# Kernel tuning notes

Hardware: AMD Instinct MI355X
Metric: run time of the kernel (lower is better)

## Reference

```python
import jax, jax.numpy as jnp
import numpy as np

D_MODEL = 1024
N_HEADS = 16
HEAD_DIM = D_MODEL // N_HEADS


def setup_inputs() -> dict:
    key = jax.random.key(0)
    k1, k2, k3 = jax.random.split(key, 3)
    x = jax.random.normal(k1, (4, 2048, D_MODEL), dtype=jnp.float32)
    # per-head qkv Linear (bias=False): torch weight [3*head_dim, d_model];
    # store transposed and stacked over heads: [H, d_model, 3*head_dim]
    w_qkv = jax.random.normal(k2, (N_HEADS, D_MODEL, 3 * HEAD_DIM), dtype=jnp.float32) * (1.0 / np.sqrt(D_MODEL))
    # output Linear (bias=False), stored transposed: [d_model, d_model]
    w_out = jax.random.normal(k3, (D_MODEL, D_MODEL), dtype=jnp.float32) * (1.0 / np.sqrt(D_MODEL))
    return {"x": x, "w_qkv": w_qkv, "w_out": w_out}


def reference(x, w_qkv, w_out):
    hd = HEAD_DIM
    # all heads' qkv in one contraction: [B, H, S, 3*hd]
    qkv = jnp.einsum("bsd,hde->bhse", x, w_qkv)
    q, k, v = qkv[..., :hd], qkv[..., hd:2 * hd], qkv[..., 2 * hd:]
    scale = 1.0 / hd  # NOTE: original scales by 1/dk, not 1/sqrt(dk)
    scores = jnp.einsum("bhqe,bhke->bhqk", q, k) * scale
    attn = jax.nn.softmax(scores, axis=-1)
    z = jnp.einsum("bhqk,bhke->bhqe", attn, v)  # [B, H, S, hd]
    # concat heads along feature dim (head order = list order)
    b, h, s, _ = z.shape
    z = jnp.transpose(z, (0, 2, 1, 3)).reshape(b, s, h * hd)
    return z @ w_out
```

## Files before the change

kernel.cpp:

```cpp
#include <hip/hip_runtime.h>
#include <hip/hip_bf16.h>

typedef unsigned short u16;
typedef __attribute__((ext_vector_type(4))) float f32x4;
typedef __attribute__((ext_vector_type(16))) float f32x16;
typedef __attribute__((ext_vector_type(8))) short s16x8;
typedef __attribute__((ext_vector_type(4))) unsigned short u16x4;

static __device__ __forceinline__ u16 f32_to_bf16(float f) {
    union { float f; unsigned u; } v; v.f = f;
    unsigned r = v.u + 0x7FFF + ((v.u >> 16) & 1);
    return (u16)(r >> 16);
}

static __device__ __forceinline__ unsigned cvt_pk_bf16(float lo, float hi) {
    unsigned r;
    asm("v_cvt_pk_bf16_f32 %0, %1, %2" : "=v"(r) : "v"(lo), "v"(hi));
    return r;
}

static __device__ __forceinline__ void pswap2(unsigned &a, unsigned &b) {
#if defined(__has_builtin) && __has_builtin(__builtin_amdgcn_permlane32_swap)
    auto r = __builtin_amdgcn_permlane32_swap(a, b, false, false);
    a = r[0]; b = r[1];
#else
    asm volatile("v_permlane32_swap_b32 %0, %1" : "+v"(a), "+v"(b));
#endif
}

static __device__ __forceinline__ float xhalf_sum(float x) {
    unsigned a = __float_as_uint(x), b = a;
    pswap2(a, b);
    return __uint_as_float(a) + __uint_as_float(b);
}

static __device__ __forceinline__ float fexp2(float x) {
#if defined(__has_builtin) && __has_builtin(__builtin_amdgcn_exp2f)
    return __builtin_amdgcn_exp2f(x);
#else
    return exp2f(x);
#endif
}

#define GLOAD_LDS16(gptr, lptr) \
    __builtin_amdgcn_global_load_lds((const __attribute__((address_space(1))) void*)(gptr), \
                                     (__attribute__((address_space(3))) void*)(lptr), 16, 0, 0)


__global__ void cvt_f32_bf16(const float* __restrict__ in, u16* __restrict__ out, int n) {
    int i = (blockIdx.x * 256 + threadIdx.x) * 4;
    if (i + 3 < n) {
        f32x4 v = *(const f32x4*)(in + i);
        u16x4 o;
        o.x = f32_to_bf16(v.x); o.y = f32_to_bf16(v.y);
        o.z = f32_to_bf16(v.z); o.w = f32_to_bf16(v.w);
        *(u16x4*)(out + i) = o;
    }
}

__global__ void cvt_wqkvT(const float* __restrict__ w, u16* __restrict__ wt) {
    int tid = blockIdx.x * 256 + threadIdx.x;
    int k = tid & 1023, n = tid >> 10;
    int h = n / 192, e = n - h * 192;
    wt[tid] = f32_to_bf16(w[(h * 1024 + k) * 192 + e]);
}

__global__ void cvt_woutT(const float* __restrict__ w, u16* __restrict__ wt) {
    int tid = blockIdx.x * 256 + threadIdx.x;
    int k = tid & 1023, n = tid >> 10;
    wt[tid] = f32_to_bf16(w[k * 1024 + n]);
}


template <int EPI>
__global__ __launch_bounds__(256, 4)
void gemm_bt(const u16* __restrict__ A, const u16* __restrict__ B,
             float* __restrict__ Cf, u16* __restrict__ Qb, u16* __restrict__ Kb,
             u16* __restrict__ Vt, int M, int N, int K) {
    __shared__ __align__(16) u16 lA[2][128 * 32];
    __shared__ __align__(16) u16 lB[2][128 * 32];

    const int t = threadIdx.x;
    const int lane = t & 63;
    const int wave = t >> 6;
    const int wr = wave >> 1, wc = wave & 1;
    const int l15 = lane & 15, g = lane >> 4;

    const int nwg = gridDim.x;
    const int cpx = nwg >> 3;
    const int orig = blockIdx.x;
    const int logical = (orig & 7) * cpx + (orig >> 3);

    const int nbx = N >> 7;
    const int bx = logical % nbx, by = logical / nbx;
    const int bm = by << 7, bn = bx << 7;

    f32x4 acc[4][4] = {};

    const int sr0 = t >> 2;
    const int ss  = t & 3;

    const u16* Abase = A + (size_t)bm * K;
    const u16* Bbase = B + (size_t)bn * K;

#define GSTAGE(buf, kt) do { \
    _Pragma("unroll") \
    for (int c = 0; c < 2; ++c) { \
        int r = sr0 + 64 * c; \
        int cl = ss ^ (r & 3); \
        GLOAD_LDS16(Abase + (size_t)r * K + (kt) + cl * 8, &lA[buf][(r * 4 + ss) * 8]); \
        GLOAD_LDS16(Bbase + (size_t)r * K + (kt) + cl * 8, &lB[buf][(r * 4 + ss) * 8]); \
    } } while (0)

    GSTAGE(0, 0);

    const int NT = K >> 5;
    for (int ti = 0; ti < NT; ++ti) {
        __syncthreads();
        if (ti + 1 < NT) GSTAGE((ti + 1) & 1, (ti + 1) << 5);

        const u16* Ac = lA[ti & 1];
        const u16* Bc = lB[ti & 1];
        s16x8 a[4], b[4];
#pragma unroll
        for (int i = 0; i < 4; ++i) {
            int r = wr * 64 + i * 16 + l15;
            int sl = g ^ (r & 3);
            a[i] = *(const s16x8*)&Ac[(r * 4 + sl) * 8];
        }
#pragma unroll
        for (int j = 0; j < 4; ++j) {
            int r = wc * 64 + j * 16 + l15;
            int sl = g ^ (r & 3);
            b[j] = *(const s16x8*)&Bc[(r * 4 + sl) * 8];
        }
#pragma unroll
        for (int i = 0; i < 4; ++i)
#pragma unroll
            for (int j = 0; j < 4; ++j)
                acc[i][j] = __builtin_amdgcn_mfma_f32_16x16x32_bf16(b[j], a[i], acc[i][j], 0, 0, 0);
    }
#undef GSTAGE

    if constexpr (EPI == 0) {
#pragma unroll
        for (int i = 0; i < 4; ++i) {
            int m = bm + wr * 64 + i * 16 + l15;
#pragma unroll
            for (int j = 0; j < 4; ++j) {
                int n0 = bn + wc * 64 + j * 16 + g * 4;
                *(f32x4*)&Cf[(size_t)m * N + n0] = acc[i][j];
            }
        }
    } else {
        const float qscale = 0.022542110013890054f;
#pragma unroll
        for (int j = 0; j < 4; ++j) {
            int n0 = bn + wc * 64 + j * 16 + g * 4;
            int h = n0 / 192;
            int e0 = n0 - h * 192;
#pragma unroll
            for (int i = 0; i < 4; ++i) {
                int m = bm + wr * 64 + i * 16 + l15;
                int bb = m >> 11, s = m & 2047;
                int bh = bb * 16 + h;
                if (e0 < 64) {
                    u16x4 q;
#pragma unroll
                    for (int r = 0; r < 4; ++r) q[r] = f32_to_bf16(acc[i][j][r] * qscale);
                    *(u16x4*)&Qb[((size_t)bh * 2048 + s) * 64 + e0] = q;
                } else if (e0 < 128) {
                    u16x4 kk;
#pragma unroll
                    for (int r = 0; r < 4; ++r) kk[r] = f32_to_bf16(acc[i][j][r]);
                    *(u16x4*)&Kb[((size_t)bh * 2048 + s) * 64 + (e0 - 64)] = kk;
                } else {
#pragma unroll
                    for (int r = 0; r < 4; ++r)
                        Vt[((size_t)bh * 64 + (e0 - 128 + r)) * 2048 + s] = f32_to_bf16(acc[i][j][r]);
                }
            }
        }
    }
}

__global__ __launch_bounds__(512, 4)
void attn32(const u16* __restrict__ Qb, const u16* __restrict__ Kb,
            const u16* __restrict__ Vt, u16* __restrict__ Zb) {
    __shared__ __align__(16) u16 lK[2][64 * 64];
    __shared__ __align__(16) u16 lV[2][64 * 64];
    __shared__ float lds_l[8][32];

    const int t = threadIdx.x;
    const int lane = t & 63;
    const int w = t >> 6;
    const int l31 = lane & 31, hi = lane >> 5;
    const int r7 = l31 & 7;

    const int orig = blockIdx.x;
    const int logical = (orig & 7) * 64 + (orig >> 3);
    const int bh = logical >> 3;
    const int qt = logical & 7;
    const int q0 = qt * 256 + w * 32;

    const u16* Kbh = Kb + (size_t)bh * 2048 * 64;
    const u16* Vbh = Vt + (size_t)bh * 64 * 2048;

    const int lr = lane >> 3;
    const int lc = (lane & 7) ^ lr;

    const u16* Qp = Qb + ((size_t)bh * 2048 + q0 + l31) * 64 + hi * 8;
    s16x8 qf[4];
#pragma unroll
    for (int kd = 0; kd < 4; ++kd) qf[kd] = *(const s16x8*)(Qp + kd * 16);

    f32x16 o0 = {}, o1 = {};
    float l = 0.f;

#define STAGE(buf, kvn) do { \
    int gr = w * 8 + lr; \
    GLOAD_LDS16(Kbh + (size_t)((kvn) + gr) * 64 + lc * 8, \
                &lK[buf][w * 512 + lane * 8]); \
    GLOAD_LDS16(Vbh + (size_t)gr * 2048 + (kvn) + lc * 8, \
                &lV[buf][w * 512 + lane * 8]); \
    } while (0)

    STAGE(0, 0);
    __syncthreads();

#pragma unroll 2
    for (int ti = 0; ti < 32; ++ti) {
        const int cur = ti & 1;
        const int kvn = ((ti + 1) & 31) * 64;

        STAGE(cur ^ 1, kvn);

        const u16* Kc = &lK[cur][0];
        f32x16 p0 = {}, p1 = {};
        __builtin_amdgcn_s_setprio(1);
#pragma unroll
        for (int kd = 0; kd < 4; ++kd) {
            int cs = ((hi + 2 * kd) ^ r7) * 8;
            s16x8 kf0 = *(const s16x8*)&Kc[l31 * 64 + cs];
            p0 = __builtin_amdgcn_mfma_f32_32x32x16_bf16(kf0, qf[kd], p0, 0, 0, 0);
            s16x8 kf1 = *(const s16x8*)&Kc[(l31 + 32) * 64 + cs];
            p1 = __builtin_amdgcn_mfma_f32_32x32x16_bf16(kf1, qf[kd], p1, 0, 0, 0);
        }
        __builtin_amdgcn_s_setprio(0);

        float rs0 = 0.f, rs1 = 0.f, rs2 = 0.f, rs3 = 0.f;
#pragma unroll
        for (int r = 0; r < 16; r += 4) {
            p0[r]     = fexp2(p0[r]);     rs0 += p0[r];
            p0[r + 1] = fexp2(p0[r + 1]); rs1 += p0[r + 1];
            p0[r + 2] = fexp2(p0[r + 2]); rs2 += p0[r + 2];
            p0[r + 3] = fexp2(p0[r + 3]); rs3 += p0[r + 3];
            p1[r]     = fexp2(p1[r]);     rs0 += p1[r];
            p1[r + 1] = fexp2(p1[r + 1]); rs1 += p1[r + 1];
            p1[r + 2] = fexp2(p1[r + 2]); rs2 += p1[r + 2];
            p1[r + 3] = fexp2(p1[r + 3]); rs3 += p1[r + 3];
        }
        l += xhalf_sum((rs0 + rs1) + (rs2 + rs3));

        union { unsigned u[8]; s16x8 v[2]; } pa0, pa1;
        {
            unsigned c0 = cvt_pk_bf16(p0[0],  p0[1]);
            unsigned c1 = cvt_pk_bf16(p0[2],  p0[3]);
            unsigned c2 = cvt_pk_bf16(p0[4],  p0[5]);
            unsigned c3 = cvt_pk_bf16(p0[6],  p0[7]);
            unsigned c4 = cvt_pk_bf16(p0[8],  p0[9]);
            unsigned c5 = cvt_pk_bf16(p0[10], p0[11]);
            unsigned c6 = cvt_pk_bf16(p0[12], p0[13]);
            unsigned c7 = cvt_pk_bf16(p0[14], p0[15]);
            pswap2(c0, c2); pswap2(c1, c3);
            pswap2(c4, c6); pswap2(c5, c7);
            pa0.u[0] = c0; pa0.u[1] = c1; pa0.u[2] = c2; pa0.u[3] = c3;
            pa0.u[4] = c4; pa0.u[5] = c5; pa0.u[6] = c6; pa0.u[7] = c7;
        }
        {
            unsigned c0 = cvt_pk_bf16(p1[0],  p1[1]);
            unsigned c1 = cvt_pk_bf16(p1[2],  p1[3]);
            unsigned c2 = cvt_pk_bf16(p1[4],  p1[5]);
            unsigned c3 = cvt_pk_bf16(p1[6],  p1[7]);
            unsigned c4 = cvt_pk_bf16(p1[8],  p1[9]);
            unsigned c5 = cvt_pk_bf16(p1[10], p1[11]);
            unsigned c6 = cvt_pk_bf16(p1[12], p1[13]);
            unsigned c7 = cvt_pk_bf16(p1[14], p1[15]);
            pswap2(c0, c2); pswap2(c1, c3);
            pswap2(c4, c6); pswap2(c5, c7);
            pa1.u[0] = c0; pa1.u[1] = c1; pa1.u[2] = c2; pa1.u[3] = c3;
            pa1.u[4] = c4; pa1.u[5] = c5; pa1.u[6] = c6; pa1.u[7] = c7;
        }

        const u16* Vc = &lV[cur][0];
        __builtin_amdgcn_s_setprio(1);
#pragma unroll
        for (int ks = 0; ks < 4; ++ks) {
            s16x8 pav = (ks < 2) ? pa0.v[ks & 1] : pa1.v[ks & 1];
            int cs = ((hi + 2 * ks) ^ r7) * 8;
            s16x8 vf0 = *(const s16x8*)&Vc[l31 * 64 + cs];
            o0 = __builtin_amdgcn_mfma_f32_32x32x16_bf16(pav, vf0, o0, 0, 0, 0);
            s16x8 vf1 = *(const s16x8*)&Vc[(l31 + 32) * 64 + cs];
            o1 = __builtin_amdgcn_mfma_f32_32x32x16_bf16(pav, vf1, o1, 0, 0, 0);
        }
        __builtin_amdgcn_s_setprio(0);

        __syncthreads();
    }
#undef STAGE

    if (lane < 32) lds_l[w][l31] = l;
    __syncthreads();

    const int b = bh >> 4, h = bh & 15;
#pragma unroll
    for (int r = 0; r < 16; ++r) {
        int qrow = (r & 3) + 8 * (r >> 2) + 4 * hi;
        float inv = 1.0f / lds_l[w][qrow];
        size_t rowbase = ((size_t)(b * 2048 + q0 + qrow)) * 1024 + h * 64 + l31;
        Zb[rowbase]      = f32_to_bf16(o0[r] * inv);
        Zb[rowbase + 32] = f32_to_bf16(o1[r] * inv);
    }
}


extern "C" void kernel_launch(void* const* d_in, const int* in_sizes, int n_in,
                              void* d_out, int out_size, void* d_ws, size_t ws_size,
                              hipStream_t stream) {
    const float* x     = (const float*)d_in[0];
    const float* w_qkv = (const float*)d_in[1];
    const float* w_out = (const float*)d_in[2];
    float* out = (float*)d_out;

    char* ws = (char*)d_ws;
    u16* xb  = (u16*)ws; ws += (size_t)8192 * 1024 * 2;
    u16* wqT = (u16*)ws; ws += (size_t)3072 * 1024 * 2;
    u16* woT = (u16*)ws; ws += (size_t)1024 * 1024 * 2;
    u16* Qb  = (u16*)ws; ws += (size_t)64 * 2048 * 64 * 2;
    u16* Kb  = (u16*)ws; ws += (size_t)64 * 2048 * 64 * 2;
    u16* Vt  = (u16*)ws; ws += (size_t)64 * 2048 * 64 * 2;
    u16* Zb  = (u16*)ws; ws += (size_t)8192 * 1024 * 2;

    cvt_f32_bf16<<<dim3(8192), dim3(256), 0, stream>>>(x, xb, 8192 * 1024);
    cvt_wqkvT<<<dim3(12288), dim3(256), 0, stream>>>(w_qkv, wqT);
    cvt_woutT<<<dim3(4096), dim3(256), 0, stream>>>(w_out, woT);

    gemm_bt<1><<<dim3(64 * 24), dim3(256), 0, stream>>>(xb, wqT, nullptr, Qb, Kb, Vt,
                                                        8192, 3072, 1024);
    attn32<<<dim3(512), dim3(512), 0, stream>>>(Qb, Kb, Vt, Zb);
    gemm_bt<0><<<dim3(64 * 8), dim3(256), 0, stream>>>(Zb, woT, out, nullptr, nullptr, nullptr,
                                                       8192, 1024, 1024);
}
```

Before: 210.6 us.

## Use 128-wide KV tiles and compute softmax row sums via ones-matrix MFMA

```diff
diff --git a/kernel.cpp b/kernel.cpp
--- a/kernel.cpp
+++ b/kernel.cpp
@@ -26,12 +26,6 @@
 #else
     asm volatile("v_permlane32_swap_b32 %0, %1" : "+v"(a), "+v"(b));
 #endif
-}
-
-static __device__ __forceinline__ float xhalf_sum(float x) {
-    unsigned a = __float_as_uint(x), b = a;
-    pswap2(a, b);
-    return __uint_as_float(a) + __uint_as_float(b);
 }
 
 static __device__ __forceinline__ float fexp2(float x) {
@@ -187,9 +181,8 @@
 __global__ __launch_bounds__(512, 4)
 void attn32(const u16* __restrict__ Qb, const u16* __restrict__ Kb,
             const u16* __restrict__ Vt, u16* __restrict__ Zb) {
-    __shared__ __align__(16) u16 lK[2][64 * 64];
-    __shared__ __align__(16) u16 lV[2][64 * 64];
-    __shared__ float lds_l[8][32];
+    __shared__ __align__(16) u16 lK[2][128 * 64];
+    __shared__ __align__(16) u16 lV[2][64 * 128];
 
     const int t = threadIdx.x;
     const int lane = t & 63;
@@ -206,118 +199,125 @@
     const u16* Kbh = Kb + (size_t)bh * 2048 * 64;
     const u16* Vbh = Vt + (size_t)bh * 64 * 2048;
 
-    const int lr = lane >> 3;
-    const int lc = (lane & 7) ^ lr;
-
     const u16* Qp = Qb + ((size_t)bh * 2048 + q0 + l31) * 64 + hi * 8;
     s16x8 qf[4];
 #pragma unroll
     for (int kd = 0; kd < 4; ++kd) qf[kd] = *(const s16x8*)(Qp + kd * 16);
 
-    f32x16 o0 = {}, o1 = {};
-    float l = 0.f;
+    s16x8 ones;
+#pragma unroll
+    for (int i = 0; i < 8; ++i) ones[i] = (short)0x3F80;
+
+    f32x16 o0 = {}, o1 = {}, ol = {};
 
 #define STAGE(buf, kvn) do { \
-    int gr = w * 8 + lr; \
-    GLOAD_LDS16(Kbh + (size_t)((kvn) + gr) * 64 + lc * 8, \
-                &lK[buf][w * 512 + lane * 8]); \
-    GLOAD_LDS16(Vbh + (size_t)gr * 2048 + (kvn) + lc * 8, \
-                &lV[buf][w * 512 + lane * 8]); \
-    } while (0)
+    _Pragma("unroll") \
+    for (int j = 0; j < 2; ++j) { \
+        int kr = w * 16 + j * 8 + (lane >> 3); \
+        GLOAD_LDS16(Kbh + (size_t)((kvn) + kr) * 64 + ((lane & 7) ^ (lane >> 3)) * 8, \
+                    &lK[buf][w * 1024 + j * 512 + lane * 8]); \
+        int vr = w * 8 + j * 4 + (lane >> 4); \
+        int vcl = (lane & 15) ^ (j * 4 + (lane >> 4)); \
+        GLOAD_LDS16(Vbh + (size_t)vr * 2048 + (kvn) + vcl * 8, \
+                    &lV[buf][w * 1024 + j * 512 + lane * 8]); \
+    } } while (0)
 
     STAGE(0, 0);
     __syncthreads();
 
 #pragma unroll 2
-    for (int ti = 0; ti < 32; ++ti) {
+    for (int ti = 0; ti < 16; ++ti) {
         const int cur = ti & 1;
-        const int kvn = ((ti + 1) & 31) * 64;
+        const int kvn = ((ti + 1) & 15) * 128;
 
         STAGE(cur ^ 1, kvn);
 
         const u16* Kc = &lK[cur][0];
-        f32x16 p0 = {}, p1 = {};
-        __builtin_amdgcn_s_setprio(1);
-#pragma unroll
-        for (int kd = 0; kd < 4; ++kd) {
-            int cs = ((hi + 2 * kd) ^ r7) * 8;
-            s16x8 kf0 = *(const s16x8*)&Kc[l31 * 64 + cs];
-            p0 = __builtin_amdgcn_mfma_f32_32x32x16_bf16(kf0, qf[kd], p0, 0, 0, 0);
-            s16x8 kf1 = *(const s16x8*)&Kc[(l31 + 32) * 64 + cs];
-            p1 = __builtin_amdgcn_mfma_f32_32x32x16_bf16(kf1, qf[kd], p1, 0, 0, 0);
-        }
-        __builtin_amdgcn_s_setprio(0);
-
-        float rs0 = 0.f, rs1 = 0.f, rs2 = 0.f, rs3 = 0.f;
-#pragma unroll
-        for (int r = 0; r < 16; r += 4) {
-            p0[r]     = fexp2(p0[r]);     rs0 += p0[r];
-            p0[r + 1] = fexp2(p0[r + 1]); rs1 += p0[r + 1];
-            p0[r + 2] = fexp2(p0[r + 2]); rs2 += p0[r + 2];
-            p0[r + 3] = fexp2(p0[r + 3]); rs3 += p0[r + 3];
-            p1[r]     = fexp2(p1[r]);     rs0 += p1[r];
-            p1[r + 1] = fexp2(p1[r + 1]); rs1 += p1[r + 1];
-            p1[r + 2] = fexp2(p1[r + 2]); rs2 += p1[r + 2];
-            p1[r + 3] = fexp2(p1[r + 3]); rs3 += p1[r + 3];
-        }
-        l += xhalf_sum((rs0 + rs1) + (rs2 + rs3));
-
-        union { unsigned u[8]; s16x8 v[2]; } pa0, pa1;
-        {
-            unsigned c0 = cvt_pk_bf16(p0[0],  p0[1]);
-            unsigned c1 = cvt_pk_bf16(p0[2],  p0[3]);
-            unsigned c2 = cvt_pk_bf16(p0[4],  p0[5]);
-            unsigned c3 = cvt_pk_bf16(p0[6],  p0[7]);
-            unsigned c4 = cvt_pk_bf16(p0[8],  p0[9]);
-            unsigned c5 = cvt_pk_bf16(p0[10], p0[11]);
-            unsigned c6 = cvt_pk_bf16(p0[12], p0[13]);
-            unsigned c7 = cvt_pk_bf16(p0[14], p0[15]);
-            pswap2(c0, c2); pswap2(c1, c3);
-            pswap2(c4, c6); pswap2(c5, c7);
-            pa0.u[0] = c0; pa0.u[1] = c1; pa0.u[2] = c2; pa0.u[3] = c3;
-            pa0.u[4] = c4; pa0.u[5] = c5; pa0.u[6] = c6; pa0.u[7] = c7;
-        }
-        {
-            unsigned c0 = cvt_pk_bf16(p1[0],  p1[1]);
-            unsigned c1 = cvt_pk_bf16(p1[2],  p1[3]);
-            unsigned c2 = cvt_pk_bf16(p1[4],  p1[5]);
-            unsigned c3 = cvt_pk_bf16(p1[6],  p1[7]);
-            unsigned c4 = cvt_pk_bf16(p1[8],  p1[9]);
-            unsigned c5 = cvt_pk_bf16(p1[10], p1[11]);
-            unsigned c6 = cvt_pk_bf16(p1[12], p1[13]);
-            unsigned c7 = cvt_pk_bf16(p1[14], p1[15]);
-            pswap2(c0, c2); pswap2(c1, c3);
-            pswap2(c4, c6); pswap2(c5, c7);
-            pa1.u[0] = c0; pa1.u[1] = c1; pa1.u[2] = c2; pa1.u[3] = c3;
-            pa1.u[4] = c4; pa1.u[5] = c5; pa1.u[6] = c6; pa1.u[7] = c7;
-        }
-
         const u16* Vc = &lV[cur][0];
-        __builtin_amdgcn_s_setprio(1);
-#pragma unroll
-        for (int ks = 0; ks < 4; ++ks) {
-            s16x8 pav = (ks < 2) ? pa0.v[ks & 1] : pa1.v[ks & 1];
-            int cs = ((hi + 2 * ks) ^ r7) * 8;
-            s16x8 vf0 = *(const s16x8*)&Vc[l31 * 64 + cs];
-            o0 = __builtin_amdgcn_mfma_f32_32x32x16_bf16(pav, vf0, o0, 0, 0, 0);
-            s16x8 vf1 = *(const s16x8*)&Vc[(l31 + 32) * 64 + cs];
-            o1 = __builtin_amdgcn_mfma_f32_32x32x16_bf16(pav, vf1, o1, 0, 0, 0);
-        }
-        __builtin_amdgcn_s_setprio(0);
+
+#pragma unroll
+        for (int hs = 0; hs < 2; ++hs) {
+            f32x16 p0 = {}, p1 = {};
+            __builtin_amdgcn_s_setprio(1);
+#pragma unroll
+            for (int kd = 0; kd < 4; ++kd) {
+                int cs = ((2 * kd + hi) ^ r7) * 8;
+                s16x8 kf0 = *(const s16x8*)&Kc[(hs * 64 + l31) * 64 + cs];
+                p0 = __builtin_amdgcn_mfma_f32_32x32x16_bf16(kf0, qf[kd], p0, 0, 0, 0);
+                s16x8 kf1 = *(const s16x8*)&Kc[(hs * 64 + l31 + 32) * 64 + cs];
+                p1 = __builtin_amdgcn_mfma_f32_32x32x16_bf16(kf1, qf[kd], p1, 0, 0, 0);
+            }
+            __builtin_amdgcn_s_setprio(0);
+
+#pragma unroll
+            for (int r = 0; r < 16; ++r) { p0[r] = fexp2(p0[r]); p1[r] = fexp2(p1[r]); }
+
+            union { unsigned u[8]; s16x8 v[2]; } pa0, pa1;
+            {
+                unsigned c0 = cvt_pk_bf16(p0[0],  p0[1]);
+                unsigned c1 = cvt_pk_bf16(p0[2],  p0[3]);
+                unsigned c2 = cvt_pk_bf16(p0[4],  p0[5]);
+                unsigned c3 = cvt_pk_bf16(p0[6],  p0[7]);
+                unsigned c4 = cvt_pk_bf16(p0[8],  p0[9]);
+                unsigned c5 = cvt_pk_bf16(p0[10], p0[11]);
+                unsigned c6 = cvt_pk_bf16(p0[12], p0[13]);
+                unsigned c7 = cvt_pk_bf16(p0[14], p0[15]);
+                pswap2(c0, c2); pswap2(c1, c3);
+                pswap2(c4, c6); pswap2(c5, c7);
+                pa0.u[0] = c0; pa0.u[1] = c1; pa0.u[2] = c2; pa0.u[3] = c3;
+                pa0.u[4] = c4; pa0.u[5] = c5; pa0.u[6] = c6; pa0.u[7] = c7;
+            }
+            __builtin_amdgcn_s_setprio(1);
+#pragma unroll
+            for (int ks = 0; ks < 2; ++ks) {
+                s16x8 pav = pa0.v[ks];
+                int cs = ((hs * 8 + ks * 2 + hi) ^ r7) * 8;
+                s16x8 vf0 = *(const s16x8*)&Vc[l31 * 128 + cs];
+                o0 = __builtin_amdgcn_mfma_f32_32x32x16_bf16(pav, vf0, o0, 0, 0, 0);
+                s16x8 vf1 = *(const s16x8*)&Vc[(l31 + 32) * 128 + cs];
+                o1 = __builtin_amdgcn_mfma_f32_32x32x16_bf16(pav, vf1, o1, 0, 0, 0);
+                ol = __builtin_amdgcn_mfma_f32_32x32x16_bf16(pav, ones, ol, 0, 0, 0);
+            }
+            __builtin_amdgcn_s_setprio(0);
+
+            {
+                unsigned c0 = cvt_pk_bf16(p1[0],  p1[1]);
+                unsigned c1 = cvt_pk_bf16(p1[2],  p1[3]);
+                unsigned c2 = cvt_pk_bf16(p1[4],  p1[5]);
+                unsigned c3 = cvt_pk_bf16(p1[6],  p1[7]);
+                unsigned c4 = cvt_pk_bf16(p1[8],  p1[9]);
+                unsigned c5 = cvt_pk_bf16(p1[10], p1[11]);
+                unsigned c6 = cvt_pk_bf16(p1[12], p1[13]);
+                unsigned c7 = cvt_pk_bf16(p1[14], p1[15]);
+                pswap2(c0, c2); pswap2(c1, c3);
+                pswap2(c4, c6); pswap2(c5, c7);
+                pa1.u[0] = c0; pa1.u[1] = c1; pa1.u[2] = c2; pa1.u[3] = c3;
+                pa1.u[4] = c4; pa1.u[5] = c5; pa1.u[6] = c6; pa1.u[7] = c7;
+            }
+            __builtin_amdgcn_s_setprio(1);
+#pragma unroll
+            for (int ks = 0; ks < 2; ++ks) {
+                s16x8 pav = pa1.v[ks];
+                int cs = ((hs * 8 + 4 + ks * 2 + hi) ^ r7) * 8;
+                s16x8 vf0 = *(const s16x8*)&Vc[l31 * 128 + cs];
+                o0 = __builtin_amdgcn_mfma_f32_32x32x16_bf16(pav, vf0, o0, 0, 0, 0);
+                s16x8 vf1 = *(const s16x8*)&Vc[(l31 + 32) * 128 + cs];
+                o1 = __builtin_amdgcn_mfma_f32_32x32x16_bf16(pav, vf1, o1, 0, 0, 0);
+                ol = __builtin_amdgcn_mfma_f32_32x32x16_bf16(pav, ones, ol, 0, 0, 0);
+            }
+            __builtin_amdgcn_s_setprio(0);
+        }
 
         __syncthreads();
     }
 #undef STAGE
 
-    if (lane < 32) lds_l[w][l31] = l;
-    __syncthreads();
-
-    const int b = bh >> 4, h = bh & 15;
+    const int bq = bh >> 4, hq = bh & 15;
 #pragma unroll
     for (int r = 0; r < 16; ++r) {
         int qrow = (r & 3) + 8 * (r >> 2) + 4 * hi;
-        float inv = 1.0f / lds_l[w][qrow];
-        size_t rowbase = ((size_t)(b * 2048 + q0 + qrow)) * 1024 + h * 64 + l31;
+        float inv = 1.0f / ol[r];
+        size_t rowbase = ((size_t)(bq * 2048 + q0 + qrow)) * 1024 + hq * 64 + l31;
         Zb[rowbase]      = f32_to_bf16(o0[r] * inv);
         Zb[rowbase + 32] = f32_to_bf16(o1[r] * inv);
     }
```

New measurement: 212.4 us. No clear change (+0.9%).

## Triple-buffer LDS staging in GEMM and attention with explicit vmcnt waits

Applied to the files above, without the earlier changes.

```diff
diff --git a/kernel.cpp b/kernel.cpp
--- a/kernel.cpp
+++ b/kernel.cpp
@@ -73,12 +73,12 @@
 
 
 template <int EPI>
-__global__ __launch_bounds__(256, 4)
+__global__ __launch_bounds__(256, 3)
 void gemm_bt(const u16* __restrict__ A, const u16* __restrict__ B,
              float* __restrict__ Cf, u16* __restrict__ Qb, u16* __restrict__ Kb,
              u16* __restrict__ Vt, int M, int N, int K) {
-    __shared__ __align__(16) u16 lA[2][128 * 32];
-    __shared__ __align__(16) u16 lB[2][128 * 32];
+    __shared__ __align__(16) u16 lA[3 * 128 * 32];
+    __shared__ __align__(16) u16 lB[3 * 128 * 32];
 
     const int t = threadIdx.x;
     const int lane = t & 63;
@@ -103,24 +103,30 @@
     const u16* Abase = A + (size_t)bm * K;
     const u16* Bbase = B + (size_t)bn * K;
 
-#define GSTAGE(buf, kt) do { \
+#define GSTAGE(bb, kt) do { \
     _Pragma("unroll") \
     for (int c = 0; c < 2; ++c) { \
         int r = sr0 + 64 * c; \
         int cl = ss ^ (r & 3); \
-        GLOAD_LDS16(Abase + (size_t)r * K + (kt) + cl * 8, &lA[buf][(r * 4 + ss) * 8]); \
-        GLOAD_LDS16(Bbase + (size_t)r * K + (kt) + cl * 8, &lB[buf][(r * 4 + ss) * 8]); \
+        GLOAD_LDS16(Abase + (size_t)r * K + (kt) + cl * 8, &lA[(bb) + (r * 4 + ss) * 8]); \
+        GLOAD_LDS16(Bbase + (size_t)r * K + (kt) + cl * 8, &lB[(bb) + (r * 4 + ss) * 8]); \
     } } while (0)
 
+    const int NT = K >> 5;
+
     GSTAGE(0, 0);
-
-    const int NT = K >> 5;
+    GSTAGE(4096, 32);
+    asm volatile("s_waitcnt vmcnt(4)" ::: "memory");
+    __builtin_amdgcn_s_barrier();
+    __builtin_amdgcn_sched_barrier(0);
+
+    int i0 = 0, i1 = 4096, i2 = 8192;
+
     for (int ti = 0; ti < NT; ++ti) {
-        __syncthreads();
-        if (ti + 1 < NT) GSTAGE((ti + 1) & 1, (ti + 1) << 5);
-
-        const u16* Ac = lA[ti & 1];
-        const u16* Bc = lB[ti & 1];
+        if (ti + 2 < NT) GSTAGE(i2, (ti + 2) << 5);
+
+        const u16* Ac = &lA[i0];
+        const u16* Bc = &lB[i0];
         s16x8 a[4], b[4];
 #pragma unroll
         for (int i = 0; i < 4; ++i) {
@@ -139,6 +145,17 @@
 #pragma unroll
             for (int j = 0; j < 4; ++j)
                 acc[i][j] = __builtin_amdgcn_mfma_f32_16x16x32_bf16(b[j], a[i], acc[i][j], 0, 0, 0);
+
+        if (ti + 1 < NT) {
+            if (ti + 2 < NT) {
+                asm volatile("s_waitcnt vmcnt(4)" ::: "memory");
+            } else {
+                asm volatile("s_waitcnt vmcnt(0)" ::: "memory");
+            }
+            __builtin_amdgcn_s_barrier();
+            __builtin_amdgcn_sched_barrier(0);
+        }
+        int tmp = i0; i0 = i1; i1 = i2; i2 = tmp;
     }
 #undef GSTAGE
 
@@ -187,8 +204,8 @@
 __global__ __launch_bounds__(512, 4)
 void attn32(const u16* __restrict__ Qb, const u16* __restrict__ Kb,
             const u16* __restrict__ Vt, u16* __restrict__ Zb) {
-    __shared__ __align__(16) u16 lK[2][64 * 64];
-    __shared__ __align__(16) u16 lV[2][64 * 64];
+    __shared__ __align__(16) u16 lK[3 * 64 * 64];
+    __shared__ __align__(16) u16 lV[3 * 64 * 64];
     __shared__ float lds_l[8][32];
 
     const int t = threadIdx.x;
@@ -217,30 +234,33 @@
     f32x16 o0 = {}, o1 = {};
     float l = 0.f;
 
-#define STAGE(buf, kvn) do { \
+#define STAGE(bb, kvn) do { \
     int gr = w * 8 + lr; \
     GLOAD_LDS16(Kbh + (size_t)((kvn) + gr) * 64 + lc * 8, \
-                &lK[buf][w * 512 + lane * 8]); \
+                &lK[(bb) + w * 512 + lane * 8]); \
     GLOAD_LDS16(Vbh + (size_t)gr * 2048 + (kvn) + lc * 8, \
-                &lV[buf][w * 512 + lane * 8]); \
+                &lV[(bb) + w * 512 + lane * 8]); \
     } while (0)
 
     STAGE(0, 0);
-    __syncthreads();
-
-#pragma unroll 2
+    STAGE(4096, 64);
+    asm volatile("s_waitcnt vmcnt(2)" ::: "memory");
+    __builtin_amdgcn_s_barrier();
+    __builtin_amdgcn_sched_barrier(0);
+
+    int i0 = 0, i1 = 4096, i2 = 8192;
+
     for (int ti = 0; ti < 32; ++ti) {
-        const int cur = ti & 1;
-        const int kvn = ((ti + 1) & 31) * 64;
-
-        STAGE(cur ^ 1, kvn);
-
-        const u16* Kc = &lK[cur][0];
+        if (ti + 2 < 32) STAGE(i2, (ti + 2) << 6);
+
+        const u16* Kc = &lK[i0];
+        const u16* Vc = &lV[i0];
+
         f32x16 p0 = {}, p1 = {};
         __builtin_amdgcn_s_setprio(1);
 #pragma unroll
         for (int kd = 0; kd < 4; ++kd) {
-            int cs = ((hi + 2 * kd) ^ r7) * 8;
+            int cs = ((2 * kd + hi) ^ r7) * 8;
             s16x8 kf0 = *(const s16x8*)&Kc[l31 * 64 + cs];
             p0 = __builtin_amdgcn_mfma_f32_32x32x16_bf16(kf0, qf[kd], p0, 0, 0, 0);
             s16x8 kf1 = *(const s16x8*)&Kc[(l31 + 32) * 64 + cs];
@@ -292,12 +312,11 @@
             pa1.u[4] = c4; pa1.u[5] = c5; pa1.u[6] = c6; pa1.u[7] = c7;
         }
 
-        const u16* Vc = &lV[cur][0];
         __builtin_amdgcn_s_setprio(1);
 #pragma unroll
         for (int ks = 0; ks < 4; ++ks) {
-            s16x8 pav = (ks < 2) ? pa0.v[ks & 1] : pa1.v[ks & 1];
-            int cs = ((hi + 2 * ks) ^ r7) * 8;
+            s16x8 pav = (ks < 2) ? pa0.v[ks] : pa1.v[ks - 2];
+            int cs = ((ks * 2 + hi) ^ r7) * 8;
             s16x8 vf0 = *(const s16x8*)&Vc[l31 * 64 + cs];
             o0 = __builtin_amdgcn_mfma_f32_32x32x16_bf16(pav, vf0, o0, 0, 0, 0);
             s16x8 vf1 = *(const s16x8*)&Vc[(l31 + 32) * 64 + cs];
@@ -305,7 +324,16 @@
         }
         __builtin_amdgcn_s_setprio(0);
 
-        __syncthreads();
+        if (ti + 1 < 32) {
+            if (ti + 2 < 32) {
+                asm volatile("s_waitcnt vmcnt(2)" ::: "memory");
+            } else {
+                asm volatile("s_waitcnt vmcnt(0)" ::: "memory");
+            }
+            __builtin_amdgcn_s_barrier();
+            __builtin_amdgcn_sched_barrier(0);
+        }
+        int tmp = i0; i0 = i1; i1 = i2; i2 = tmp;
     }
 #undef STAGE
 
```

After: 207.7 us. No clear change (-1.4%).
